# Kernel tuning notes

Hardware: AMD Instinct MI355X
Metric: run time of the kernel (lower is better)

Reference implementation:

```python
import jax, jax.numpy as jnp
import numpy as np

V = 32000   # vocab_size
D = 1024    # dim
NH = 16     # n_heads
HD = 64     # head_dim
L = 2       # n_layers
E = 8       # n_experts
K = 2       # n_active_experts
H = 2048    # expert_dim
B = 2
T = 1024
EPS = 1e-6
THETA = 10000.0
STD = 0.02


def rmsnorm(x, w):
    rms = jax.lax.rsqrt(jnp.mean(x * x, axis=-1, keepdims=True) + EPS)
    return x * rms * w


def rope_cos_sin(t_len):
    inv = 1.0 / (THETA ** (jnp.arange(0, HD, 2, dtype=jnp.float32) / HD))
    t = jnp.arange(t_len, dtype=jnp.float32)
    f = jnp.outer(t, inv)  # [T, HD//2]
    return jnp.cos(f), jnp.sin(f)


def apply_rope(x, cos, sin):
    # x: [B, T, NH, HD]; complex rotation on interleaved (even, odd) pairs
    xr = x[..., 0::2]
    xi = x[..., 1::2]
    c = cos[None, :, None, :]
    s = sin[None, :, None, :]
    out_r = xr * c - xi * s
    out_i = xr * s + xi * c
    return jnp.stack([out_r, out_i], axis=-1).reshape(x.shape)


def setup_inputs() -> dict:
    key = jax.random.key(0)
    ks = jax.random.split(key, 13)
    n = lambda k, shp: (jax.random.normal(k, shp, dtype=jnp.float32) * STD)
    return {
        "tokens": jax.random.randint(ks[0], (B, T), 0, V, dtype=jnp.int64)
                   if jax.config.jax_enable_x64 else
                   jax.random.randint(ks[0], (B, T), 0, V, dtype=jnp.int32),
        "emb": n(ks[1], (V, D)),            # tied embedding / output projection
        "attn_norm_w": jnp.ones((L, D), jnp.float32),
        "wq": n(ks[2], (L, D, D)),
        "wk": n(ks[3], (L, D, D)),
        "wv": n(ks[4], (L, D, D)),
        "wo": n(ks[5], (L, D, D)),
        "ffn_norm_w": jnp.ones((L, D), jnp.float32),
        "gate_w": n(ks[6], (L, D, E)),
        "w1": n(ks[7], (L, E, D, H)),
        "w2": n(ks[8], (L, E, H, D)),
        "w3": n(ks[9], (L, E, D, H)),
        "final_norm_w": jnp.ones((D,), jnp.float32),
    }


def reference(tokens, emb, attn_norm_w, wq, wk, wv, wo, ffn_norm_w,
              gate_w, w1, w2, w3, final_norm_w):
    b, t = tokens.shape
    h = emb[tokens]                                     # [B,T,D]
    cos, sin = rope_cos_sin(t)
    mask = jnp.where(jnp.tril(jnp.ones((t, t), bool)), 0.0, -jnp.inf)
    scale = 1.0 / np.sqrt(HD).astype(np.float32)
    aux_total = jnp.float32(0.0)

    for l in range(L):
        x = h
        # --- attention ---
        hn = rmsnorm(x, attn_norm_w[l])
        q = (hn @ wq[l]).reshape(b, t, NH, HD)
        k = (hn @ wk[l]).reshape(b, t, NH, HD)
        v = (hn @ wv[l]).reshape(b, t, NH, HD)
        q = apply_rope(q, cos, sin)
        k = apply_rope(k, cos, sin)
        scores = jnp.einsum('bqhd,bkhd->bhqk', q, k) * scale + mask
        attn = jax.nn.softmax(scores, axis=-1)
        o = jnp.einsum('bhqk,bkhd->bqhd', attn, v).reshape(b, t, D) @ wo[l]
        x = x + o
        # --- MoE ---
        xf = rmsnorm(x, ffn_norm_w[l]).reshape(-1, D)   # [N,D]
        gate_logits = xf @ gate_w[l]                    # [N,E]
        probs = jax.nn.softmax(gate_logits, axis=-1)
        vals, idx = jax.lax.top_k(probs, K)             # [N,K]
        w = vals / (jnp.sum(vals, axis=-1, keepdims=True) + 1e-8)
        oh = jax.nn.one_hot(idx, E, dtype=jnp.float32)  # [N,K,E]
        combine = jnp.sum(oh * w[..., None], axis=1)    # [N,E]
        tokens_per_expert = oh.sum(axis=1).mean(axis=0)
        aux_total = aux_total + E * jnp.sum(tokens_per_expert * probs.mean(axis=0))
        h1 = jnp.einsum('nd,edh->neh', xf, w1[l])
        h3 = jnp.einsum('nd,edh->neh', xf, w3[l])
        eo = jnp.einsum('neh,ehd->ned', jax.nn.silu(h1) * h3, w2[l])
        moe_out = jnp.einsum('ned,ne->nd', eo, combine).reshape(b, t, D)
        h = x + moe_out

    logits = rmsnorm(h, final_norm_w) @ emb.T           # [B,T,V]
    return logits, aux_total
```

## Files before the change

### kernel.cpp

```cpp
#include <hip/hip_runtime.h>
#include <hip/hip_bf16.h>
#include <math.h>

#define D_MODEL 1024
#define NHEADS  16
#define HDIM    64
#define NEXP    8
#define FFH     2048
#define BATCH   2
#define SEQ     1024
#define NTOK    2048
#define VOCAB   32000
#define LDSS    40

typedef __attribute__((ext_vector_type(4))) float f32x4;
typedef __attribute__((ext_vector_type(2))) float f32x2;
typedef __attribute__((ext_vector_type(8))) _Float16 f16x8;
typedef __attribute__((ext_vector_type(4))) unsigned short u16x4;

#define TIER    4.8828125e-4f
#define DESCALE 2.44140625e-4f
#define INV_S   0.015625f
#define INV_M   7.62939453125e-6f

__device__ __forceinline__ unsigned short f2h(float x) {
    _Float16 h = (_Float16)x;
    union { _Float16 h; unsigned short u; } v; v.h = h; return v.u;
}
__device__ __forceinline__ float h2f(unsigned short u) {
    union { unsigned short u; _Float16 h; } v; v.u = u; return (float)v.h;
}
__device__ __forceinline__ void split2h(float x, unsigned short& h, unsigned short& m) {
    _Float16 hf = (_Float16)(x * 64.f);
    union { _Float16 h; unsigned short u; } a; a.h = hf;
    h = a.u;
    float r = x - (float)hf * INV_S;
    _Float16 mf = (_Float16)(r * 131072.f);
    union { _Float16 h; unsigned short u; } b; b.h = mf;
    m = b.u;
}

#define MFMAH(a, b, c) __builtin_amdgcn_mfma_f32_16x16x32_f16((a), (b), (c), 0, 0, 0)

#define PSA ((long)NTOK * D_MODEL)
#define PSW ((long)D_MODEL * D_MODEL)

__global__ __launch_bounds__(256) void rmsnorm_kernel(const float* __restrict__ x,
    const float* __restrict__ wt, unsigned short* __restrict__ out2)
{
    __shared__ float red[4];
    int n = blockIdx.x;
    int c = threadIdx.x << 2;
    f32x4 v = *(const f32x4*)(x + (long)n*D_MODEL + c);
    float ss = v.x*v.x + v.y*v.y + v.z*v.z + v.w*v.w;
    #pragma unroll
    for (int dd = 32; dd; dd >>= 1) ss += __shfl_xor(ss, dd);
    if ((threadIdx.x & 63) == 0) red[threadIdx.x >> 6] = ss;
    __syncthreads();
    float tot = red[0] + red[1] + red[2] + red[3];
    float rms = rsqrtf(tot * (1.f / D_MODEL) + 1e-6f);
    f32x4 wv = *(const f32x4*)(wt + c);
    f32x4 o = v * rms;
    o = o * wv;
    u16x4 hv, mv;
    #pragma unroll
    for (int j = 0; j < 4; j++) { unsigned short h,m; split2h(o[j],h,m); hv[j]=h; mv[j]=m; }
    long idx = (long)n*D_MODEL + c;
    *(u16x4*)(out2 + 0*PSA + idx) = hv;
    *(u16x4*)(out2 + 1*PSA + idx) = mv;
}

__global__ __launch_bounds__(256) void wsplitT_kernel(
    const float* __restrict__ wqs, const float* __restrict__ wks, const float* __restrict__ wvs,
    unsigned short* __restrict__ oq, unsigned short* __restrict__ ok, unsigned short* __restrict__ ov)
{
    __shared__ float t[64][65];
    int k0 = blockIdx.x*64, n0 = blockIdx.y*64, z = blockIdx.z;
    const float* src = (z==0) ? wqs : (z==1) ? wks : wvs;
    unsigned short* dst = (z==0) ? oq : (z==1) ? ok : ov;
    int tid = threadIdx.x;
    int a = tid & 63, g = tid >> 6;
    #pragma unroll 4
    for (int i = 0; i < 16; i++) {
        int k = g*16 + i;
        t[k][a] = src[(long)(k0+k)*D_MODEL + n0 + a];
    }
    __syncthreads();
    #pragma unroll 4
    for (int i = 0; i < 16; i++) {
        int n = g*16 + i;
        float v = t[a][n];
        unsigned short h,m; split2h(v,h,m);
        long idx = (long)(n0+n)*D_MODEL + k0 + a;
        dst[0*PSW + idx] = h;
        dst[1*PSW + idx] = m;
    }
}

__global__ __launch_bounds__(256, 6) void qkv_kernel(
    const unsigned short* __restrict__ A2,
    const unsigned short* __restrict__ Wq2, const unsigned short* __restrict__ Wk2,
    const unsigned short* __restrict__ Wv2,
    float* __restrict__ qf, float* __restrict__ kf, float* __restrict__ vf)
{
    __shared__ __align__(16) unsigned short As[2][64*LDSS];
    __shared__ __align__(16) unsigned short Bs[2][64*LDSS];
    int z = blockIdx.z;
    const unsigned short* B2 = (z==0) ? Wq2 : (z==1) ? Wk2 : Wv2;
    float* out = (z==0) ? qf : (z==1) ? kf : vf;
    int n0 = blockIdx.x*64, m0 = blockIdx.y*64;
    int tid = threadIdx.x, w = tid >> 6, lane = tid & 63;
    int wm = (w >> 1)*32, wn = (w & 1)*32;
    int lr = lane & 15, lg = lane >> 4;
    f32x4 zero = {0.f,0.f,0.f,0.f};
    f32x4 a0[2][2], a1[2][2];
    #pragma unroll
    for (int mi = 0; mi < 2; mi++)
        #pragma unroll
        for (int ni = 0; ni < 2; ni++) { a0[mi][ni] = zero; a1[mi][ni] = zero; }
    int rb = tid >> 3, kc = (tid & 7) << 2;

    for (int k0 = 0; k0 < D_MODEL; k0 += 32) {
        #pragma unroll
        for (int p = 0; p < 2; p++) {
            int r = p*32 + rb;
            #pragma unroll
            for (int s = 0; s < 2; s++) {
                *(u16x4*)&As[s][r*LDSS + kc] = *(const u16x4*)(A2 + s*PSA + (long)(m0+r)*D_MODEL + k0 + kc);
                *(u16x4*)&Bs[s][r*LDSS + kc] = *(const u16x4*)(B2 + s*PSW + (long)(n0+r)*D_MODEL + k0 + kc);
            }
        }
        __syncthreads();
        f16x8 bh[2], bm[2];
        #pragma unroll
        for (int ni = 0; ni < 2; ni++) {
            bh[ni] = *(const f16x8*)&Bs[0][(wn + ni*16 + lr)*LDSS + lg*8];
            bm[ni] = *(const f16x8*)&Bs[1][(wn + ni*16 + lr)*LDSS + lg*8];
        }
        #pragma unroll
        for (int mi = 0; mi < 2; mi++) {
            f16x8 ah = *(const f16x8*)&As[0][(wm + mi*16 + lr)*LDSS + lg*8];
            f16x8 am = *(const f16x8*)&As[1][(wm + mi*16 + lr)*LDSS + lg*8];
            #pragma unroll
            for (int ni = 0; ni < 2; ni++) {
                a0[mi][ni] = MFMAH(ah, bh[ni], a0[mi][ni]);
                a1[mi][ni] = MFMAH(ah, bm[ni], a1[mi][ni]);
                a1[mi][ni] = MFMAH(am, bh[ni], a1[mi][ni]);
            }
        }
        __syncthreads();
    }
    #pragma unroll
    for (int mi = 0; mi < 2; mi++)
        #pragma unroll
        for (int r = 0; r < 4; r++) {
            long row = m0 + wm + mi*16 + lg*4 + r;
            #pragma unroll
            for (int ni = 0; ni < 2; ni++) {
                int col = n0 + wn + ni*16 + lr;
                out[row*D_MODEL + col] = (a0[mi][ni][r] + a1[mi][ni][r]*TIER) * DESCALE;
            }
        }
}

__global__ __launch_bounds__(256, 3) void wo_kernel(
    const float* __restrict__ A, const float* __restrict__ B, float* h)
{
    __shared__ __align__(16) unsigned short As[2][64*LDSS];
    __shared__ __align__(16) unsigned short Bs[2][64*LDSS];
    int n0 = blockIdx.x*64, m0 = blockIdx.y*64;
    int tid = threadIdx.x, w = tid >> 6, lane = tid & 63;
    int wm = (w >> 1)*32, wn = (w & 1)*32;
    int lr = lane & 15, lg = lane >> 4;
    f32x4 zero = {0.f,0.f,0.f,0.f};
    f32x4 a0[2][2], a1[2][2];
    #pragma unroll
    for (int mi = 0; mi < 2; mi++)
        #pragma unroll
        for (int ni = 0; ni < 2; ni++) { a0[mi][ni] = zero; a1[mi][ni] = zero; }
    int rb = tid >> 3, kc = (tid & 7) << 2;
    int nb = (tid & 31) << 1, kb = (tid >> 5) << 2;

    f32x4 pAv[2];
    f32x2 pBv[4];
    #pragma unroll
    for (int p = 0; p < 2; p++)
        pAv[p] = *(const f32x4*)(A + (long)(m0 + p*32 + rb)*D_MODEL + kc);
    #pragma unroll
    for (int i = 0; i < 4; i++)
        pBv[i] = *(const f32x2*)(B + (long)(kb + i)*D_MODEL + n0 + nb);

    for (int k0 = 0; k0 < D_MODEL; k0 += 32) {
        int kn = k0 + 32;
        #pragma unroll
        for (int p = 0; p < 2; p++) {
            int r = p*32 + rb;
            u16x4 hv, mv;
            #pragma unroll
            for (int j = 0; j < 4; j++) { unsigned short hh,mm; split2h(pAv[p][j],hh,mm); hv[j]=hh; mv[j]=mm; }
            *(u16x4*)&As[0][r*LDSS + kc] = hv;
            *(u16x4*)&As[1][r*LDSS + kc] = mv;
        }
        #pragma unroll
        for (int i = 0; i < 2; i++) {
            int r = nb + i;
            u16x4 hv, mv;
            unsigned short hh,mm;
            split2h(pBv[0][i],hh,mm); hv[0]=hh; mv[0]=mm;
            split2h(pBv[1][i],hh,mm); hv[1]=hh; mv[1]=mm;
            split2h(pBv[2][i],hh,mm); hv[2]=hh; mv[2]=mm;
            split2h(pBv[3][i],hh,mm); hv[3]=hh; mv[3]=mm;
            *(u16x4*)&Bs[0][r*LDSS + kb] = hv;
            *(u16x4*)&Bs[1][r*LDSS + kb] = mv;
        }
        if (kn < D_MODEL) {
            #pragma unroll
            for (int p = 0; p < 2; p++)
                pAv[p] = *(const f32x4*)(A + (long)(m0 + p*32 + rb)*D_MODEL + kn + kc);
            #pragma unroll
            for (int i = 0; i < 4; i++)
                pBv[i] = *(const f32x2*)(B + (long)(kn + kb + i)*D_MODEL + n0 + nb);
        }
        __syncthreads();
        f16x8 bh[2], bm[2];
        #pragma unroll
        for (int ni = 0; ni < 2; ni++) {
            bh[ni] = *(const f16x8*)&Bs[0][(wn + ni*16 + lr)*LDSS + lg*8];
            bm[ni] = *(const f16x8*)&Bs[1][(wn + ni*16 + lr)*LDSS + lg*8];
        }
        #pragma unroll
        for (int mi = 0; mi < 2; mi++) {
            f16x8 ah = *(const f16x8*)&As[0][(wm + mi*16 + lr)*LDSS + lg*8];
            f16x8 am = *(const f16x8*)&As[1][(wm + mi*16 + lr)*LDSS + lg*8];
            #pragma unroll
            for (int ni = 0; ni < 2; ni++) {
                a0[mi][ni] = MFMAH(ah, bh[ni], a0[mi][ni]);
                a1[mi][ni] = MFMAH(ah, bm[ni], a1[mi][ni]);
                a1[mi][ni] = MFMAH(am, bh[ni], a1[mi][ni]);
            }
        }
        __syncthreads();
    }
    #pragma unroll
    for (int mi = 0; mi < 2; mi++)
        #pragma unroll
        for (int r = 0; r < 4; r++) {
            long row = m0 + wm + mi*16 + lg*4 + r;
            #pragma unroll
            for (int ni = 0; ni < 2; ni++) {
                int col = n0 + wn + ni*16 + lr;
                h[row*D_MODEL + col] += (a0[mi][ni][r] + a1[mi][ni][r]*TIER) * DESCALE;
            }
        }
}

template<int SPL>
__global__ __launch_bounds__(256, 3) void moe13_kernel(
    const unsigned short* __restrict__ A2, const float* __restrict__ W1,
    const float* __restrict__ W3, float* __restrict__ G,
    const int* __restrict__ rowidx, const int* __restrict__ counts,
    const int* __restrict__ offsets)
{
    __shared__ __align__(16) unsigned short As[SPL][64*LDSS];
    __shared__ __align__(16) unsigned short Bs[SPL][128*LDSS];
    const int P1 = (SPL == 2) ? 1 : 0;
    int e = blockIdx.z;
    int cnt = counts[e], off = offsets[e];
    int n0 = blockIdx.x*128, m0 = blockIdx.y*64;
    if (m0 >= cnt) return;
    int tid = threadIdx.x, w = tid >> 6, lane = tid & 63;
    int wm = (w >> 1)*32, wn = (w & 1)*64;
    int lr = lane & 15, lg = lane >> 4;
    int rb = tid >> 3, kc = (tid & 7) << 2;
    f32x4 zero = {0.f,0.f,0.f,0.f};

    long arow[2]; int av[2];
    #pragma unroll
    for (int p = 0; p < 2; p++) {
        int r = p*32 + rb;
        av[p] = (m0 + r < cnt) ? 1 : 0;
        arow[p] = av[p] ? (long)rowidx[off + m0 + r] : 0;
    }
    u16x4 z4 = {0,0,0,0};
    f32x4 sl[2][4];

    #pragma unroll
    for (int mat = 0; mat < 2; mat++) {
        const float* bp = (mat ? W3 : W1) + (long)e * (D_MODEL*FFH);
        f32x4 a0[2][4], a1t[2][4];
        #pragma unroll
        for (int mi = 0; mi < 2; mi++)
            #pragma unroll
            for (int ni = 0; ni < 4; ni++) { a0[mi][ni] = zero; a1t[mi][ni] = zero; }

        for (int k0 = 0; k0 < D_MODEL; k0 += 32) {
            #pragma unroll
            for (int p = 0; p < 2; p++) {
                int r = p*32 + rb;
                #pragma unroll
                for (int s = 0; s < SPL; s++)
                    *(u16x4*)&As[s][r*LDSS + kc] = av[p] ?
                        *(const u16x4*)(A2 + s*PSA + arow[p]*D_MODEL + k0 + kc) : z4;
            }
            f32x4 c0 = *(const f32x4*)(bp + (long)(k0+kc+0)*FFH + n0 + rb*4);
            f32x4 c1 = *(const f32x4*)(bp + (long)(k0+kc+1)*FFH + n0 + rb*4);
            f32x4 c2 = *(const f32x4*)(bp + (long)(k0+kc+2)*FFH + n0 + rb*4);
            f32x4 c3 = *(const f32x4*)(bp + (long)(k0+kc+3)*FFH + n0 + rb*4);
            #pragma unroll
            for (int i = 0; i < 4; i++) {
                int r = rb*4 + i;
                if (SPL == 2) {
                    u16x4 hv, mv;
                    unsigned short hh,mm;
                    split2h(c0[i],hh,mm); hv[0]=hh; mv[0]=mm;
                    split2h(c1[i],hh,mm); hv[1]=hh; mv[1]=mm;
                    split2h(c2[i],hh,mm); hv[2]=hh; mv[2]=mm;
                    split2h(c3[i],hh,mm); hv[3]=hh; mv[3]=mm;
                    *(u16x4*)&Bs[0][r*LDSS + kc] = hv;
                    *(u16x4*)&Bs[P1][r*LDSS + kc] = mv;
                } else {
                    u16x4 hv = {f2h(c0[i]), f2h(c1[i]), f2h(c2[i]), f2h(c3[i])};
                    *(u16x4*)&Bs[0][r*LDSS + kc] = hv;
                }
            }
            __syncthreads();
            f16x8 bh[4], bm[4];
            #pragma unroll
            for (int ni = 0; ni < 4; ni++) {
                bh[ni] = *(const f16x8*)&Bs[0][(wn + ni*16 + lr)*LDSS + lg*8];
                if (SPL == 2) bm[ni] = *(const f16x8*)&Bs[P1][(wn + ni*16 + lr)*LDSS + lg*8];
            }
            #pragma unroll
            for (int mi = 0; mi < 2; mi++) {
                f16x8 ah = *(const f16x8*)&As[0][(wm + mi*16 + lr)*LDSS + lg*8];
                #pragma unroll
                for (int ni = 0; ni < 4; ni++) {
                    a0[mi][ni] = MFMAH(ah, bh[ni], a0[mi][ni]);
                    if (SPL == 2) {
                        f16x8 am = *(const f16x8*)&As[P1][(wm + mi*16 + lr)*LDSS + lg*8];
                        a1t[mi][ni] = MFMAH(ah, bm[ni], a1t[mi][ni]);
                        a1t[mi][ni] = MFMAH(am, bh[ni], a1t[mi][ni]);
                    }
                }
            }
            __syncthreads();
        }
        if (mat == 0) {
            #pragma unroll
            for (int mi = 0; mi < 2; mi++)
                #pragma unroll
                for (int ni = 0; ni < 4; ni++) {
                    f32x4 v = (SPL == 2) ? (a0[mi][ni] + a1t[mi][ni]*TIER)*DESCALE
                                         : a0[mi][ni]*INV_S;
                    #pragma unroll
                    for (int r = 0; r < 4; r++) {
                        float s = v[r];
                        v[r] = s / (1.f + expf(-s));
                    }
                    sl[mi][ni] = v;
                }
        } else {
            #pragma unroll
            for (int mi = 0; mi < 2; mi++)
                #pragma unroll
                for (int r = 0; r < 4; r++) {
                    int rowl = wm + mi*16 + lg*4 + r;
                    if (m0 + rowl < cnt) {
                        long crow = off + m0 + rowl;
                        #pragma unroll
                        for (int ni = 0; ni < 4; ni++) {
                            int col = n0 + wn + ni*16 + lr;
                            float v3 = (SPL == 2) ? (a0[mi][ni][r] + a1t[mi][ni][r]*TIER)*DESCALE
                                                  : a0[mi][ni][r]*INV_S;
                            G[crow*FFH + col] = sl[mi][ni][r] * v3;
                        }
                    }
                }
        }
    }
}

template<int SPL>
__global__ __launch_bounds__(256, 4) void w2_kernel(
    const float* __restrict__ G, const float* __restrict__ W2, float* h,
    const int* __restrict__ rowidx, const float* __restrict__ wrow,
    const int* __restrict__ counts, const int* __restrict__ offsets)
{
    __shared__ __align__(16) unsigned short As[SPL][64*LDSS];
    __shared__ __align__(16) unsigned short Bs[SPL][64*LDSS];
    const int P1 = (SPL == 2) ? 1 : 0;
    int e = blockIdx.z;
    int cnt = counts[e], off = offsets[e];
    int n0 = blockIdx.x*64, m0 = blockIdx.y*64;
    if (m0 >= cnt) return;
    const float* bp = W2 + (long)e * (FFH*D_MODEL);
    int tid = threadIdx.x, w = tid >> 6, lane = tid & 63;
    int wm = (w >> 1)*32, wn = (w & 1)*32;
    int lr = lane & 15, lg = lane >> 4;
    f32x4 zero = {0.f,0.f,0.f,0.f};
    f32x4 a0[2][2], a1[2][2];
    #pragma unroll
    for (int mi = 0; mi < 2; mi++)
        #pragma unroll
        for (int ni = 0; ni < 2; ni++) { a0[mi][ni] = zero; a1[mi][ni] = zero; }
    int rb = tid >> 3, kc = (tid & 7) << 2;
    int nb = (tid & 31) << 1, kb = (tid >> 5) << 2;

    int av[2];
    #pragma unroll
    for (int p = 0; p < 2; p++) av[p] = (m0 + p*32 + rb < cnt) ? 1 : 0;
    f32x4 pG[2];
    f32x2 pW[4];
    #pragma unroll
    for (int p = 0; p < 2; p++)
        pG[p] = av[p] ? *(const f32x4*)(G + (long)(off + m0 + p*32 + rb)*FFH + kc) : zero;
    #pragma unroll
    for (int i = 0; i < 4; i++)
        pW[i] = *(const f32x2*)(bp + (long)(kb + i)*D_MODEL + n0 + nb);

    for (int k0 = 0; k0 < FFH; k0 += 32) {
        int kn = k0 + 32;
        #pragma unroll
        for (int p = 0; p < 2; p++) {
            int r = p*32 + rb;
            if (SPL == 2) {
                u16x4 hv, mv;
                #pragma unroll
                for (int j = 0; j < 4; j++) { unsigned short hh,mm; split2h(pG[p][j],hh,mm); hv[j]=hh; mv[j]=mm; }
                *(u16x4*)&As[0][r*LDSS + kc] = hv;
                *(u16x4*)&As[P1][r*LDSS + kc] = mv;
            } else {
                u16x4 hv;
                #pragma unroll
                for (int j = 0; j < 4; j++) hv[j] = f2h(pG[p][j]);
                *(u16x4*)&As[0][r*LDSS + kc] = hv;
            }
        }
        #pragma unroll
        for (int i = 0; i < 2; i++) {
            int r = nb + i;
            if (SPL == 2) {
                u16x4 hv, mv;
                unsigned short hh,mm;
                split2h(pW[0][i],hh,mm); hv[0]=hh; mv[0]=mm;
                split2h(pW[1][i],hh,mm); hv[1]=hh; mv[1]=mm;
                split2h(pW[2][i],hh,mm); hv[2]=hh; mv[2]=mm;
                split2h(pW[3][i],hh,mm); hv[3]=hh; mv[3]=mm;
                *(u16x4*)&Bs[0][r*LDSS + kb] = hv;
                *(u16x4*)&Bs[P1][r*LDSS + kb] = mv;
            } else {
                u16x4 hv = {f2h(pW[0][i]), f2h(pW[1][i]), f2h(pW[2][i]), f2h(pW[3][i])};
                *(u16x4*)&Bs[0][r*LDSS + kb] = hv;
            }
        }
        if (kn < FFH) {
            #pragma unroll
            for (int p = 0; p < 2; p++)
                pG[p] = av[p] ? *(const f32x4*)(G + (long)(off + m0 + p*32 + rb)*FFH + kn + kc) : zero;
            #pragma unroll
            for (int i = 0; i < 4; i++)
                pW[i] = *(const f32x2*)(bp + (long)(kn + kb + i)*D_MODEL + n0 + nb);
        }
        __syncthreads();
        f16x8 bh[2], bm[2];
        #pragma unroll
        for (int ni = 0; ni < 2; ni++) {
            bh[ni] = *(const f16x8*)&Bs[0][(wn + ni*16 + lr)*LDSS + lg*8];
            if (SPL == 2) bm[ni] = *(const f16x8*)&Bs[P1][(wn + ni*16 + lr)*LDSS + lg*8];
        }
        #pragma unroll
        for (int mi = 0; mi < 2; mi++) {
            f16x8 ah = *(const f16x8*)&As[0][(wm + mi*16 + lr)*LDSS + lg*8];
            #pragma unroll
            for (int ni = 0; ni < 2; ni++) {
                a0[mi][ni] = MFMAH(ah, bh[ni], a0[mi][ni]);
                if (SPL == 2) {
                    f16x8 am = *(const f16x8*)&As[P1][(wm + mi*16 + lr)*LDSS + lg*8];
                    a1[mi][ni] = MFMAH(ah, bm[ni], a1[mi][ni]);
                    a1[mi][ni] = MFMAH(am, bh[ni], a1[mi][ni]);
                }
            }
        }
        __syncthreads();
    }
    #pragma unroll
    for (int mi = 0; mi < 2; mi++)
        #pragma unroll
        for (int r = 0; r < 4; r++) {
            int rowl = wm + mi*16 + lg*4 + r;
            if (m0 + rowl < cnt) {
                long crow = off + m0 + rowl;
                long n = rowidx[crow];
                float wgt = wrow[crow];
                #pragma unroll
                for (int ni = 0; ni < 2; ni++) {
                    int col = n0 + wn + ni*16 + lr;
                    float val = (SPL == 2) ? (a0[mi][ni][r] + a1[mi][ni][r]*TIER)*DESCALE
                                           : a0[mi][ni][r];
                    atomicAdd(&h[n*D_MODEL + col], wgt * val);
                }
            }
        }
}

__global__ __launch_bounds__(256, 3) void attn_kernel(
    const float* __restrict__ q, const float* __restrict__ k,
    const float* __restrict__ v, float* __restrict__ att)
{
    __shared__ __align__(16) unsigned short Qs[2][64*72];
    __shared__ __align__(16) unsigned short KP[2][2560];
    __shared__ __align__(16) unsigned short Vt[2][2560];

    int qt = blockIdx.x, bh = blockIdx.y;
    int b = bh >> 4, hh = bh & 15;
    int tid = threadIdx.x, w = tid >> 6, lane = tid & 63;
    int lr = lane & 15, lg = lane >> 4;
    int lrow = tid >> 4;
    int lcol = (tid & 15) << 2;

    const float* qbase = q + ((long)(b*SEQ + qt*64) * D_MODEL + hh*64);
    #pragma unroll
    for (int p = 0; p < 4; p++) {
        int r = p*16 + lrow;
        f32x4 vv = *(const f32x4*)(qbase + (long)r * D_MODEL + lcol);
        #pragma unroll
        for (int jj = 0; jj < 4; jj++) {
            unsigned short hh2,mm2; split2h(vv[jj],hh2,mm2);
            Qs[0][r*72 + lcol + jj] = hh2;
            Qs[1][r*72 + lcol + jj] = mm2;
        }
    }

    f32x4 zero = {0.f,0.f,0.f,0.f};
    f32x4 o0[4] = {zero, zero, zero, zero};
    f32x4 o1[4] = {zero, zero, zero, zero};
    float mrun[4] = {-INFINITY,-INFINITY,-INFINITY,-INFINITY};
    float lrun[4] = {0.f,0.f,0.f,0.f};

    int ntile = 2*qt + 2;
    for (int jt = 0; jt < ntile; jt++) {
        const float* kbase = k + ((long)(b*SEQ + jt*32) * D_MODEL + hh*64);
        const float* vbase = v + ((long)(b*SEQ + jt*32) * D_MODEL + hh*64);
        #pragma unroll
        for (int p = 0; p < 2; p++) {
            int r = p*16 + lrow;
            f32x4 kv4 = *(const f32x4*)(kbase + (long)r * D_MODEL + lcol);
            f32x4 vv4 = *(const f32x4*)(vbase + (long)r * D_MODEL + lcol);
            #pragma unroll
            for (int jj = 0; jj < 4; jj++) {
                unsigned short hh2,mm2;
                split2h(kv4[jj],hh2,mm2);
                KP[0][r*72 + lcol + jj] = hh2;
                KP[1][r*72 + lcol + jj] = mm2;
                split2h(vv4[jj],hh2,mm2);
                Vt[0][(lcol+jj)*40 + r] = hh2;
                Vt[1][(lcol+jj)*40 + r] = mm2;
            }
        }
        __syncthreads();

        f32x4 s0[2] = {zero, zero};
        f32x4 s1[2] = {zero, zero};
        #pragma unroll
        for (int ks = 0; ks < 2; ks++) {
            f16x8 qh = *(const f16x8*)&Qs[0][(w*16 + lr)*72 + ks*32 + lg*8];
            f16x8 qm = *(const f16x8*)&Qs[1][(w*16 + lr)*72 + ks*32 + lg*8];
            #pragma unroll
            for (int ni = 0; ni < 2; ni++) {
                f16x8 kh = *(const f16x8*)&KP[0][(ni*16 + lr)*72 + ks*32 + lg*8];
                f16x8 km = *(const f16x8*)&KP[1][(ni*16 + lr)*72 + ks*32 + lg*8];
                s0[ni] = MFMAH(qh, kh, s0[ni]);
                s1[ni] = MFMAH(qh, km, s1[ni]);
                s1[ni] = MFMAH(qm, kh, s1[ni]);
            }
        }
        __syncthreads();

        #pragma unroll
        for (int r = 0; r < 4; r++) {
            int qg = qt*64 + w*16 + lg*4 + r;
            float sv[2];
            float mx = -INFINITY;
            #pragma unroll
            for (int ni = 0; ni < 2; ni++) {
                int kg = jt*32 + ni*16 + lr;
                float val = (s0[ni][r] + s1[ni][r]*TIER) * (0.125f * DESCALE);
                if (kg > qg) val = -INFINITY;
                sv[ni] = val;
                mx = fmaxf(mx, val);
            }
            #pragma unroll
            for (int dd = 1; dd < 16; dd <<= 1)
                mx = fmaxf(mx, __shfl_xor(mx, dd));
            float mnew  = fmaxf(mrun[r], mx);
            float alpha = expf(mrun[r] - mnew);
            float ps = 0.f;
            #pragma unroll
            for (int ni = 0; ni < 2; ni++) {
                float pv = expf(sv[ni] - mnew);
                sv[ni] = pv;
                ps += pv;
            }
            #pragma unroll
            for (int dd = 1; dd < 16; dd <<= 1)
                ps += __shfl_xor(ps, dd);
            lrun[r] = lrun[r] * alpha + ps;
            mrun[r] = mnew;
            #pragma unroll
            for (int d = 0; d < 4; d++) { o0[d][r] *= alpha; o1[d][r] *= alpha; }
            int prow = w*16 + lg*4 + r;
            #pragma unroll
            for (int ni = 0; ni < 2; ni++) {
                unsigned short hh2,mm2; split2h(sv[ni],hh2,mm2);
                KP[0][prow*40 + ni*16 + lr] = hh2;
                KP[1][prow*40 + ni*16 + lr] = mm2;
            }
        }
        {
            f16x8 ph = *(const f16x8*)&KP[0][(w*16 + lr)*40 + lg*8];
            f16x8 pm = *(const f16x8*)&KP[1][(w*16 + lr)*40 + lg*8];
            #pragma unroll
            for (int ni = 0; ni < 4; ni++) {
                f16x8 vh = *(const f16x8*)&Vt[0][(ni*16 + lr)*40 + lg*8];
                f16x8 vm = *(const f16x8*)&Vt[1][(ni*16 + lr)*40 + lg*8];
                o0[ni] = MFMAH(ph, vh, o0[ni]);
                o1[ni] = MFMAH(ph, vm, o1[ni]);
                o1[ni] = MFMAH(pm, vh, o1[ni]);
            }
        }
        __syncthreads();
    }
    float* obase = att + ((long)(b*SEQ + qt*64) * D_MODEL + hh*64);
    #pragma unroll
    for (int r = 0; r < 4; r++) {
        float inv = DESCALE / lrun[r];
        #pragma unroll
        for (int ni = 0; ni < 4; ni++)
            obase[(long)(w*16 + lg*4 + r) * D_MODEL + ni*16 + lr] =
                (o0[ni][r] + o1[ni][r]*TIER) * inv;
    }
}

__global__ __launch_bounds__(256) void logits_kernel(
    const unsigned short* __restrict__ A0, const float* __restrict__ Bmat, float* __restrict__ C)
{
    __shared__ __align__(16) unsigned short As[128*LDSS];
    __shared__ __align__(16) unsigned short Bs[128*LDSS];
    int flat = blockIdx.y * 16 + blockIdx.x;
    int wid  = (flat & 7) * 500 + (flat >> 3);
    int m0 = (wid & 15) * 128;
    int n0 = (wid >> 4) * 128;
    int tid = threadIdx.x, w = tid >> 6, lane = tid & 63;
    int wm = (w >> 1)*64, wn = (w & 1)*64;
    int lr = lane & 15, lg = lane >> 4;
    f32x4 zero = {0.f,0.f,0.f,0.f};
    f32x4 acc[4][4];
    #pragma unroll
    for (int mi = 0; mi < 4; mi++)
        #pragma unroll
        for (int ni = 0; ni < 4; ni++) acc[mi][ni] = zero;
    int rb = tid >> 3, kc = (tid & 7) << 2;
    for (int k0 = 0; k0 < D_MODEL; k0 += 32) {
        #pragma unroll
        for (int p = 0; p < 4; p++) {
            int r = p*32 + rb;
            *(u16x4*)&As[r*LDSS + kc] = *(const u16x4*)(A0 + (long)(m0+r)*D_MODEL + k0 + kc);
            f32x4 vv = *(const f32x4*)(Bmat + (long)(n0+r)*D_MODEL + k0 + kc);
            u16x4 hv;
            #pragma unroll
            for (int j = 0; j < 4; j++) hv[j] = f2h(vv[j]);
            *(u16x4*)&Bs[r*LDSS + kc] = hv;
        }
        __syncthreads();
        f16x8 bfv[4], af[4];
        #pragma unroll
        for (int ni = 0; ni < 4; ni++)
            bfv[ni] = *(const f16x8*)&Bs[(wn + ni*16 + lr)*LDSS + lg*8];
        #pragma unroll
        for (int mi = 0; mi < 4; mi++)
            af[mi] = *(const f16x8*)&As[(wm + mi*16 + lr)*LDSS + lg*8];
        #pragma unroll
        for (int mi = 0; mi < 4; mi++)
            #pragma unroll
            for (int ni = 0; ni < 4; ni++)
                acc[mi][ni] = MFMAH(af[mi], bfv[ni], acc[mi][ni]);
        __syncthreads();
    }
    #pragma unroll
    for (int mi = 0; mi < 4; mi++)
        #pragma unroll
        for (int r = 0; r < 4; r++) {
            long row = m0 + wm + mi*16 + lg*4 + r;
            #pragma unroll
            for (int ni = 0; ni < 4; ni++) {
                int col = n0 + wn + ni*16 + lr;
                C[row*VOCAB + col] = acc[mi][ni][r] * INV_S;
            }
        }
}

__global__ __launch_bounds__(256) void embed_kernel(const int* __restrict__ tok,
    const float* __restrict__ emb, float* __restrict__ h)
{
    int n = blockIdx.x;
    int c = threadIdx.x << 2;
    long t = tok[n];
    *(f32x4*)(h + (long)n*D_MODEL + c) = *(const f32x4*)(emb + t*D_MODEL + c);
}

__global__ __launch_bounds__(256) void ropetab_kernel(float* __restrict__ tab)
{
    int idx = blockIdx.x * 256 + threadIdx.x;
    if (idx >= SEQ * 32) return;
    int t = idx >> 5, i = idx & 31;
    double inv = pow(10000.0, -(double)(2*i) / 64.0);
    double ang = (double)t * inv;
    tab[idx*2]   = (float)cos(ang);
    tab[idx*2+1] = (float)sin(ang);
}

__global__ __launch_bounds__(256) void rope_kernel(float* __restrict__ q, float* __restrict__ kk,
    const float* __restrict__ tab)
{
    int gid = blockIdx.x * 256 + threadIdx.x;
    if (gid >= NTOK * 512) return;
    int n   = gid >> 9;
    int rem = gid & 511;
    int hh  = rem >> 5;
    int i   = rem & 31;
    int t   = n & (SEQ - 1);
    float cs = tab[(t*32 + i)*2];
    float sn = tab[(t*32 + i)*2 + 1];
    long base = (long)n * D_MODEL + hh*64 + 2*i;
    float qr = q[base], qi = q[base+1];
    q[base]   = qr*cs - qi*sn;
    q[base+1] = qr*sn + qi*cs;
    float kr = kk[base], ki = kk[base+1];
    kk[base]   = kr*cs - ki*sn;
    kk[base+1] = kr*sn + ki*cs;
}

__global__ __launch_bounds__(64) void gate_kernel(const unsigned short* __restrict__ xf2,
    const float* __restrict__ gw, int* __restrict__ counts,
    int* __restrict__ eid, float* __restrict__ wts, float* __restrict__ pbuf)
{
    int n = blockIdx.x;
    int lane = threadIdx.x;
    float acc[8] = {0,0,0,0,0,0,0,0};
    for (int d0 = lane*4; d0 < D_MODEL; d0 += 256) {
        long idx = (long)n*D_MODEL + d0;
        u16x4 xh = *(const u16x4*)(xf2 + 0*PSA + idx);
        u16x4 xm = *(const u16x4*)(xf2 + 1*PSA + idx);
        #pragma unroll
        for (int j = 0; j < 4; j++) {
            float xv = h2f(xh[j])*INV_S + h2f(xm[j])*INV_M;
            const float* g = gw + (d0+j) * 8;
            #pragma unroll
            for (int e = 0; e < 8; e++) acc[e] += xv * g[e];
        }
    }
    #pragma unroll
    for (int e = 0; e < 8; e++) {
        #pragma unroll
        for (int dd = 32; dd; dd >>= 1) acc[e] += __shfl_xor(acc[e], dd);
    }
    if (lane == 0) {
        float mx = acc[0];
        #pragma unroll
        for (int e = 1; e < 8; e++) mx = fmaxf(mx, acc[e]);
        float pe[8], ssum = 0.f;
        #pragma unroll
        for (int e = 0; e < 8; e++) { pe[e] = expf(acc[e] - mx); ssum += pe[e]; }
        float sinv = 1.f / ssum;
        #pragma unroll
        for (int e = 0; e < 8; e++) { pe[e] *= sinv; pbuf[n*8 + e] = pe[e]; }
        int e1 = 0;
        #pragma unroll
        for (int e = 1; e < 8; e++) if (pe[e] > pe[e1]) e1 = e;
        int e2 = -1;
        #pragma unroll
        for (int e = 0; e < 8; e++) if (e != e1 && (e2 < 0 || pe[e] > pe[e2])) e2 = e;
        float v1 = pe[e1], v2 = pe[e2];
        float wsum = v1 + v2 + 1e-8f;
        eid[n*2] = e1; eid[n*2+1] = e2;
        wts[n*2] = v1 / wsum; wts[n*2+1] = v2 / wsum;
        atomicAdd(counts + e1, 1);
        atomicAdd(counts + e2, 1);
    }
}

__global__ __launch_bounds__(64) void scan_kernel(const int* __restrict__ counts,
    int* __restrict__ offs, int* __restrict__ cursor,
    const float* __restrict__ pbuf, float* __restrict__ aux)
{
    int t = threadIdx.x;
    int e = t & 7, c = t >> 3;
    float s = 0.f;
    for (int n = 0; n < NTOK/8; n++)
        s += pbuf[(c*(NTOK/8) + n)*8 + e];
    #pragma unroll
    for (int dd = 8; dd < 64; dd <<= 1) s += __shfl_xor(s, dd);
    __shared__ float red[8];
    if (t < 8) red[t] = s;
    __syncthreads();
    if (t == 0) {
        int o = 0; float a = 0.f;
        for (int kk = 0; kk < 8; kk++) {
            offs[kk] = o; cursor[kk] = o; o += counts[kk];
            a += (float)counts[kk] * red[kk];
        }
        aux[0] += 8.f * a / ((float)NTOK * (float)NTOK);
    }
}

__global__ __launch_bounds__(256) void assign_kernel(const int* __restrict__ eid,
    const float* __restrict__ wts, int* __restrict__ cursor,
    int* __restrict__ rowidx, float* __restrict__ wrow)
{
    int n = blockIdx.x * 256 + threadIdx.x;
    if (n >= NTOK) return;
    #pragma unroll
    for (int s = 0; s < 2; s++) {
        int e = eid[n*2 + s];
        int p = atomicAdd(cursor + e, 1);
        rowidx[p] = n;
        wrow[p] = wts[n*2 + s];
    }
}

__global__ void write_aux_kernel(float* __restrict__ out, const float* __restrict__ aux)
{
    if (threadIdx.x == 0 && blockIdx.x == 0)
        out[(long)NTOK * VOCAB] = aux[0];
}

extern "C" void kernel_launch(void* const* d_in, const int* in_sizes, int n_in,
                              void* d_out, int out_size, void* d_ws, size_t ws_size,
                              hipStream_t stream)
{
    const int*   tokens = (const int*)d_in[0];
    const float* emb    = (const float*)d_in[1];
    const float* anw    = (const float*)d_in[2];
    const float* wq     = (const float*)d_in[3];
    const float* wk     = (const float*)d_in[4];
    const float* wv     = (const float*)d_in[5];
    const float* wo     = (const float*)d_in[6];
    const float* fnw    = (const float*)d_in[7];
    const float* gw     = (const float*)d_in[8];
    const float* w1     = (const float*)d_in[9];
    const float* w2     = (const float*)d_in[10];
    const float* w3     = (const float*)d_in[11];
    const float* finw   = (const float*)d_in[12];
    float* out = (float*)d_out;

    char* W = (char*)d_ws;
    const size_t MB = 1024u * 1024u;
    int*   counts = (int*)(W + 0);
    int*   offs   = (int*)(W + 64);
    int*   cursor = (int*)(W + 128);
    float* aux    = (float*)(W + 192);
    int*   eid    = (int*)(W + 4096);
    float* wts    = (float*)(W + 4096 + 16384);
    int*   rowix  = (int*)(W + 4096 + 32768);
    float* wrow   = (float*)(W + 4096 + 49152);
    float* pbuf   = (float*)(W + 4096 + 65536);
    float* rtab   = (float*)(W + 4096 + 131072 + 65536);
    float*          h    = (float*)(W + 1*MB);
    unsigned short* hn2  = (unsigned short*)(W + 9*MB);
    float*          qf   = (float*)(W + 17*MB);
    float*          kf   = (float*)(W + 25*MB);
    float*          vf   = (float*)(W + 33*MB);
    unsigned short* wq2  = (unsigned short*)(W + 41*MB);
    unsigned short* wk2  = (unsigned short*)(W + 45*MB);
    unsigned short* wv2  = (unsigned short*)(W + 49*MB);
    float*          att  = (float*)(W + 41*MB);
    float*          g    = (float*)(W + 17*MB);

    hipMemsetAsync(W, 0, 256, stream);
    ropetab_kernel<<<(SEQ*32 + 255)/256, 256, 0, stream>>>(rtab);
    embed_kernel<<<NTOK, 256, 0, stream>>>(tokens, emb, h);

    for (int l = 0; l < 2; l++) {
        const float* wql = wq + (size_t)l*D_MODEL*D_MODEL;
        const float* wkl = wk + (size_t)l*D_MODEL*D_MODEL;
        const float* wvl = wv + (size_t)l*D_MODEL*D_MODEL;
        const float* wol = wo + (size_t)l*D_MODEL*D_MODEL;

        rmsnorm_kernel<<<NTOK, 256, 0, stream>>>(h, anw + (size_t)l*D_MODEL, hn2);
        wsplitT_kernel<<<dim3(16, 16, 3), 256, 0, stream>>>(wql, wkl, wvl, wq2, wk2, wv2);
        qkv_kernel<<<dim3(D_MODEL/64, NTOK/64, 3), 256, 0, stream>>>(hn2, wq2, wk2, wv2, qf, kf, vf);
        rope_kernel<<<(NTOK*512 + 255)/256, 256, 0, stream>>>(qf, kf, rtab);
        attn_kernel<<<dim3(SEQ/64, BATCH*NHEADS), 256, 0, stream>>>(qf, kf, vf, att);
        wo_kernel<<<dim3(D_MODEL/64, NTOK/64), 256, 0, stream>>>(att, wol, h);

        rmsnorm_kernel<<<NTOK, 256, 0, stream>>>(h, fnw + (size_t)l*D_MODEL, hn2);
        hipMemsetAsync(W, 0, 160, stream);
        gate_kernel<<<NTOK, 64, 0, stream>>>(hn2, gw + (size_t)l*D_MODEL*NEXP, counts, eid, wts, pbuf);
        scan_kernel<<<1, 64, 0, stream>>>(counts, offs, cursor, pbuf, aux);
        assign_kernel<<<(NTOK + 255)/256, 256, 0, stream>>>(eid, wts, cursor, rowix, wrow);

        const float* w1l = w1 + (size_t)l*NEXP*D_MODEL*FFH;
        const float* w3l = w3 + (size_t)l*NEXP*D_MODEL*FFH;
        const float* w2l = w2 + (size_t)l*NEXP*FFH*D_MODEL;
        dim3 g13(FFH/128, 2*NTOK/64, NEXP);
        dim3 g2d(D_MODEL/64, 2*NTOK/64, NEXP);
        if (l == 0) {
            moe13_kernel<2><<<g13, 256, 0, stream>>>(hn2, w1l, w3l, g, rowix, counts, offs);
            w2_kernel<2><<<g2d, 256, 0, stream>>>(g, w2l, h, rowix, wrow, counts, offs);
        } else {
            moe13_kernel<1><<<g13, 256, 0, stream>>>(hn2, w1l, w3l, g, rowix, counts, offs);
            w2_kernel<1><<<g2d, 256, 0, stream>>>(g, w2l, h, rowix, wrow, counts, offs);
        }
    }

    rmsnorm_kernel<<<NTOK, 256, 0, stream>>>(h, finw, hn2);
    logits_kernel<<<dim3(NTOK/128, VOCAB/128), 256, 0, stream>>>(hn2, emb, out);
    write_aux_kernel<<<1, 1, 0, stream>>>(out, aux);
}
```

Before: 1.744 ms.

## Pre-convert embedding to fp16 and add swizzled fp16 logits GEMM

Adds a pass that converts the fp32 embedding table to fp16 in workspace once per call. The logits GEMM then reads fp16 B tiles directly, with no per-tile conversion, and uses a remapped block order meant to improve L2 reuse. This path is taken only when the workspace is at least 120 MB. It also raises the occupancy hint for the SPL==1 moe13 instantiation. The cost is an extra full read of the fp32 embedding plus a write of the fp16 copy, set against the repeated fp32 B loads across the 16 M-tiles in the original logits kernel.

```diff
diff --git a/kernel.cpp b/kernel.cpp
--- a/kernel.cpp
+++ b/kernel.cpp
@@ -68,6 +68,19 @@
     long idx = (long)n*D_MODEL + c;
     *(u16x4*)(out2 + 0*PSA + idx) = hv;
     *(u16x4*)(out2 + 1*PSA + idx) = mv;
+}
+
+__global__ __launch_bounds__(256) void emb2h_kernel(const float* __restrict__ emb,
+    unsigned short* __restrict__ out)
+{
+    long i = (long)blockIdx.x * 2048 + (long)threadIdx.x * 8;
+    f32x4 v0 = *(const f32x4*)(emb + i);
+    f32x4 v1 = *(const f32x4*)(emb + i + 4);
+    u16x4 h0, h1;
+    #pragma unroll
+    for (int j = 0; j < 4; j++) { h0[j] = f2h(v0[j]); h1[j] = f2h(v1[j]); }
+    *(u16x4*)(out + i)     = h0;
+    *(u16x4*)(out + i + 4) = h1;
 }
 
 __global__ __launch_bounds__(256) void wsplitT_kernel(
@@ -255,7 +268,7 @@
 }
 
 template<int SPL>
-__global__ __launch_bounds__(256, 3) void moe13_kernel(
+__global__ __launch_bounds__(256, (SPL == 1) ? 4 : 3) void moe13_kernel(
     const unsigned short* __restrict__ A2, const float* __restrict__ W1,
     const float* __restrict__ W3, float* __restrict__ G,
     const int* __restrict__ rowidx, const int* __restrict__ counts,
@@ -670,6 +683,60 @@
             #pragma unroll
             for (int j = 0; j < 4; j++) hv[j] = f2h(vv[j]);
             *(u16x4*)&Bs[r*LDSS + kc] = hv;
+        }
+        __syncthreads();
+        f16x8 bfv[4], af[4];
+        #pragma unroll
+        for (int ni = 0; ni < 4; ni++)
+            bfv[ni] = *(const f16x8*)&Bs[(wn + ni*16 + lr)*LDSS + lg*8];
+        #pragma unroll
+        for (int mi = 0; mi < 4; mi++)
+            af[mi] = *(const f16x8*)&As[(wm + mi*16 + lr)*LDSS + lg*8];
+        #pragma unroll
+        for (int mi = 0; mi < 4; mi++)
+            #pragma unroll
+            for (int ni = 0; ni < 4; ni++)
+                acc[mi][ni] = MFMAH(af[mi], bfv[ni], acc[mi][ni]);
+        __syncthreads();
+    }
+    #pragma unroll
+    for (int mi = 0; mi < 4; mi++)
+        #pragma unroll
+        for (int r = 0; r < 4; r++) {
+            long row = m0 + wm + mi*16 + lg*4 + r;
+            #pragma unroll
+            for (int ni = 0; ni < 4; ni++) {
+                int col = n0 + wn + ni*16 + lr;
+                C[row*VOCAB + col] = acc[mi][ni][r] * INV_S;
+            }
+        }
+}
+
+__global__ __launch_bounds__(256) void logits_h_kernel(
+    const unsigned short* __restrict__ A0, const unsigned short* __restrict__ Bh, float* __restrict__ C)
+{
+    __shared__ __align__(16) unsigned short As[128*LDSS];
+    __shared__ __align__(16) unsigned short Bs[128*LDSS];
+    int flat = blockIdx.y * 16 + blockIdx.x;
+    int wid  = (flat & 7) * 500 + (flat >> 3);
+    int m0 = (wid & 15) * 128;
+    int n0 = (wid >> 4) * 128;
+    int tid = threadIdx.x, w = tid >> 6, lane = tid & 63;
+    int wm = (w >> 1)*64, wn = (w & 1)*64;
+    int lr = lane & 15, lg = lane >> 4;
+    f32x4 zero = {0.f,0.f,0.f,0.f};
+    f32x4 acc[4][4];
+    #pragma unroll
+    for (int mi = 0; mi < 4; mi++)
+        #pragma unroll
+        for (int ni = 0; ni < 4; ni++) acc[mi][ni] = zero;
+    int rb = tid >> 3, kc = (tid & 7) << 2;
+    for (int k0 = 0; k0 < D_MODEL; k0 += 32) {
+        #pragma unroll
+        for (int p = 0; p < 4; p++) {
+            int r = p*32 + rb;
+            *(u16x4*)&As[r*LDSS + kc] = *(const u16x4*)(A0 + (long)(m0+r)*D_MODEL + k0 + kc);
+            *(u16x4*)&Bs[r*LDSS + kc] = *(const u16x4*)(Bh + (long)(n0+r)*D_MODEL + k0 + kc);
         }
         __syncthreads();
         f16x8 bfv[4], af[4];
@@ -875,10 +942,15 @@
     unsigned short* wv2  = (unsigned short*)(W + 49*MB);
     float*          att  = (float*)(W + 41*MB);
     float*          g    = (float*)(W + 17*MB);
+    unsigned short* embh = (unsigned short*)(W + 53*MB);
+
+    const bool use_embh = ws_size >= (size_t)120 * MB;
 
     hipMemsetAsync(W, 0, 256, stream);
     ropetab_kernel<<<(SEQ*32 + 255)/256, 256, 0, stream>>>(rtab);
     embed_kernel<<<NTOK, 256, 0, stream>>>(tokens, emb, h);
+    if (use_embh)
+        emb2h_kernel<<<(int)(((long)VOCAB*D_MODEL)/2048), 256, 0, stream>>>(emb, embh);
 
     for (int l = 0; l < 2; l++) {
         const float* wql = wq + (size_t)l*D_MODEL*D_MODEL;
@@ -914,6 +986,9 @@
     }
 
     rmsnorm_kernel<<<NTOK, 256, 0, stream>>>(h, finw, hn2);
-    logits_kernel<<<dim3(NTOK/128, VOCAB/128), 256, 0, stream>>>(hn2, emb, out);
+    if (use_embh)
+        logits_h_kernel<<<dim3(NTOK/128, VOCAB/128), 256, 0, stream>>>(hn2, embh, out);
+    else
+        logits_kernel<<<dim3(NTOK/128, VOCAB/128), 256, 0, stream>>>(hn2, emb, out);
     write_aux_kernel<<<1, 1, 0, stream>>>(out, aux);
 }
```

Measured after the change: 1.758 ms. Within noise of the previous version (+0.8%).
